# Performance work log

Measured on AMD Instinct MI355X. Metric: run time of the kernel, lower is better.

The kernel has to match this reference:

```python
import jax, jax.numpy as jnp
import numpy as np

N = 50000      # nodes
E = 800000     # edges (avg degree 16)
IN, HID, OUT = 128, 128, 64


def setup_inputs() -> dict:
    key = jax.random.key(0)
    ks = jax.random.split(key, 8)
    x = jax.random.normal(ks[0], (N, IN), dtype=jnp.float32)
    edge_index = jax.random.randint(ks[1], (2, E), 0, N, dtype=jnp.int64)
    s1 = 1.0 / np.sqrt(IN)
    s2 = 1.0 / np.sqrt(HID)
    # SAGEConv params: lin_l acts on aggregated neighbors (has bias), lin_r on root
    W1l = jax.random.uniform(ks[2], (IN, HID), jnp.float32, -s1, s1)
    W1r = jax.random.uniform(ks[3], (IN, HID), jnp.float32, -s1, s1)
    b1 = jax.random.uniform(ks[4], (HID,), jnp.float32, -s1, s1)
    W2l = jax.random.uniform(ks[5], (HID, OUT), jnp.float32, -s2, s2)
    W2r = jax.random.uniform(ks[6], (HID, OUT), jnp.float32, -s2, s2)
    b2 = jax.random.uniform(ks[7], (OUT,), jnp.float32, -s2, s2)
    return {"x": x, "edge_index": edge_index, "W1l": W1l, "W1r": W1r,
            "b1": b1, "W2l": W2l, "W2r": W2r, "b2": b2}


def reference(x, edge_index, W1l, W1r, b1, W2l, W2r, b2):
    src = edge_index[0]
    dst = edge_index[1]
    n = x.shape[0]
    deg = jax.ops.segment_sum(jnp.ones(src.shape, x.dtype), dst, num_segments=n)
    inv_deg = (1.0 / jnp.maximum(deg, 1.0))[:, None]  # [N,1], avoid div-by-zero

    def mean_agg(h):
        # gather neighbor feats, scatter-sum to destination, normalize by in-degree
        return jax.ops.segment_sum(h[src], dst, num_segments=n) * inv_deg

    # SAGEConv layer 1: lin_l(mean_j x_j) + lin_r(x_i), then ReLU (dropout off in eval)
    h = mean_agg(x) @ W1l + x @ W1r + b1
    h = jax.nn.relu(h)
    # SAGEConv layer 2
    out = mean_agg(h) @ W2l + h @ W2r + b2
    return out
```

## Files before the change

kernel.cpp:

```cpp
#include <hip/hip_runtime.h>
#include <hip/hip_bf16.h>


typedef __attribute__((ext_vector_type(8))) short bf16x8;
typedef __attribute__((ext_vector_type(4))) float f32x4;

__device__ __forceinline__ ushort f2b(float f) {
    uint u = __float_as_uint(f);
    return (ushort)((u + 0x7fffu + ((u >> 16) & 1u)) >> 16);
}
__device__ __forceinline__ float b2f(ushort h) { return __uint_as_float(((uint)h) << 16); }
__device__ __forceinline__ float blo(uint u) { return __uint_as_float(u << 16); }
__device__ __forceinline__ float bhi(uint u) { return __uint_as_float(u & 0xffff0000u); }

__global__ void count_deg_k(const int* __restrict__ dstv, int* __restrict__ cnt, int E) {
    int e = blockIdx.x * blockDim.x + threadIdx.x;
    if (e < E) atomicAdd(&cnt[dstv[e]], 1);
}

__global__ __launch_bounds__(256) void blocksum_k(const int* __restrict__ cnt,
                                                  int* __restrict__ bsum, int n) {
    __shared__ int red[4];
    int b = blockIdx.x, t = threadIdx.x;
    int base = b * 1024 + t * 4;
    int s = 0;
    #pragma unroll
    for (int i = 0; i < 4; ++i) { int idx = base + i; if (idx < n) s += cnt[idx]; }
    #pragma unroll
    for (int off = 32; off > 0; off >>= 1) s += __shfl_down(s, off);
    if ((t & 63) == 0) red[t >> 6] = s;
    __syncthreads();
    if (t == 0) bsum[b] = red[0] + red[1] + red[2] + red[3];
}

__global__ __launch_bounds__(256) void bscan_k(int* __restrict__ bsum, int nb) {
    __shared__ int sd[256];
    int t = threadIdx.x;
    int v = (t < nb) ? bsum[t] : 0;
    sd[t] = v;
    __syncthreads();
    for (int off = 1; off < 256; off <<= 1) {
        int u = (t >= off) ? sd[t - off] : 0;
        __syncthreads();
        sd[t] += u;
        __syncthreads();
    }
    if (t < nb) bsum[t] = sd[t] - v;
}

__global__ __launch_bounds__(256) void scanout_k(const int* __restrict__ cnt,
                                                 const int* __restrict__ bbase,
                                                 int* __restrict__ rowptr,
                                                 int* __restrict__ pos,
                                                 float* __restrict__ inv_deg,
                                                 int n, int E) {
    __shared__ int sums[256];
    int b = blockIdx.x, t = threadIdx.x;
    int base = b * 1024 + t * 4;
    int v[4];
    int s = 0;
    #pragma unroll
    for (int i = 0; i < 4; ++i) {
        int idx = base + i;
        v[i] = (idx < n) ? cnt[idx] : 0;
        s += v[i];
    }
    sums[t] = s;
    __syncthreads();
    for (int off = 1; off < 256; off <<= 1) {
        int u = (t >= off) ? sums[t - off] : 0;
        __syncthreads();
        sums[t] += u;
        __syncthreads();
    }
    int pre = sums[t] - s + bbase[b];
    #pragma unroll
    for (int i = 0; i < 4; ++i) {
        int idx = base + i;
        if (idx < n) {
            rowptr[idx] = pre;
            pos[idx] = pre;
            inv_deg[idx] = 1.0f / (float)max(v[i], 1);
            pre += v[i];
        }
    }
    if (b == 0 && t == 0) rowptr[n] = E;
}

__global__ void fill_k(const int* __restrict__ srcv, const int* __restrict__ dstv,
                       int* __restrict__ pos, int* __restrict__ csr, int E) {
    int e = blockIdx.x * blockDim.x + threadIdx.x;
    if (e < E) {
        int p = atomicAdd(&pos[dstv[e]], 1);
        csr[p] = srcv[e];
    }
}

__global__ void castx_k(const float* __restrict__ x, ushort* __restrict__ xb, int total4) {
    int i = blockIdx.x * blockDim.x + threadIdx.x;
    if (i < total4) {
        float4 v = reinterpret_cast<const float4*>(x)[i];
        ushort4 r;
        r.x = f2b(v.x); r.y = f2b(v.y); r.z = f2b(v.z); r.w = f2b(v.w);
        reinterpret_cast<ushort4*>(xb)[i] = r;
    }
}

__global__ void prepw_k(const float* __restrict__ W1l, const float* __restrict__ W1r,
                        const float* __restrict__ W2l, const float* __restrict__ W2r,
                        ushort* __restrict__ w1lt, ushort* __restrict__ w1rt,
                        ushort* __restrict__ w2lt, ushort* __restrict__ w2rt) {
    int i = blockIdx.x * blockDim.x + threadIdx.x;
    if (i < 16384) {
        int nn = i >> 7, k = i & 127;
        w1lt[i] = f2b(W1l[k * 128 + nn]);
    } else if (i < 32768) {
        int j = i - 16384, nn = j >> 7, k = j & 127;
        w1rt[j] = f2b(W1r[k * 128 + nn]);
    } else if (i < 40960) {
        int j = i - 32768, nn = j >> 7, k = j & 127;
        w2lt[j] = f2b(W2l[k * 64 + nn]);
    } else if (i < 49152) {
        int j = i - 40960, nn = j >> 7, k = j & 127;
        w2rt[j] = f2b(W2r[k * 64 + nn]);
    }
}

template<int F>
__global__ __launch_bounds__(256) void aggb_k(const ushort* __restrict__ feat,
                                              const int* __restrict__ rowptr,
                                              const int* __restrict__ csr,
                                              const float* __restrict__ invd,
                                              ushort* __restrict__ out, int n) {
    int tid = blockIdx.x * 256 + threadIdx.x;
    int node = tid >> 5;
    int sl = threadIdx.x & 31;
    if (node >= n) return;
    int s = rowptr[node], e = rowptr[node + 1];
    float sc = invd[node];
    if (F == 128) {
        float a0 = 0, a1 = 0, a2 = 0, a3 = 0;
        int p = s;
        for (; p + 2 <= e; p += 2) {
            int u0 = csr[p], u1 = csr[p + 1];
            uint2 v0 = *reinterpret_cast<const uint2*>(&feat[(size_t)u0 * 128 + sl * 4]);
            uint2 v1 = *reinterpret_cast<const uint2*>(&feat[(size_t)u1 * 128 + sl * 4]);
            a0 += blo(v0.x); a1 += bhi(v0.x); a2 += blo(v0.y); a3 += bhi(v0.y);
            a0 += blo(v1.x); a1 += bhi(v1.x); a2 += blo(v1.y); a3 += bhi(v1.y);
        }
        if (p < e) {
            uint2 v0 = *reinterpret_cast<const uint2*>(&feat[(size_t)csr[p] * 128 + sl * 4]);
            a0 += blo(v0.x); a1 += bhi(v0.x); a2 += blo(v0.y); a3 += bhi(v0.y);
        }
        ushort4 r;
        r.x = f2b(a0 * sc); r.y = f2b(a1 * sc); r.z = f2b(a2 * sc); r.w = f2b(a3 * sc);
        *reinterpret_cast<ushort4*>(&out[(size_t)node * 128 + sl * 4]) = r;
    } else {
        float a0 = 0, a1 = 0;
        int p = s;
        for (; p + 2 <= e; p += 2) {
            int u0 = csr[p], u1 = csr[p + 1];
            uint v0 = *reinterpret_cast<const uint*>(&feat[(size_t)u0 * 64 + sl * 2]);
            uint v1 = *reinterpret_cast<const uint*>(&feat[(size_t)u1 * 64 + sl * 2]);
            a0 += blo(v0) + blo(v1); a1 += bhi(v0) + bhi(v1);
        }
        if (p < e) {
            uint v0 = *reinterpret_cast<const uint*>(&feat[(size_t)csr[p] * 64 + sl * 2]);
            a0 += blo(v0); a1 += bhi(v0);
        }
        ushort2 r;
        r.x = f2b(a0 * sc); r.y = f2b(a1 * sc);
        *reinterpret_cast<ushort2*>(&out[(size_t)node * 64 + sl * 2]) = r;
    }
}

template<int NC, int NSRC, bool RELU, bool OUT_BF16, bool HAS_BIAS, bool HAS_ADD>
__global__ __launch_bounds__(256) void mgemm_k(const ushort* __restrict__ A0,
                                               const ushort* __restrict__ B0,
                                               const ushort* __restrict__ A1,
                                               const ushort* __restrict__ B1,
                                               const ushort* __restrict__ addm,
                                               const float* __restrict__ bias,
                                               void* __restrict__ Cout, int n) {
    constexpr int AST = 136;
    __shared__ ushort At[64 * AST];
    __shared__ ushort Bt[NC * AST];
    int t = threadIdx.x;
    int brow = blockIdx.x * 64;
    int w = t >> 6, l = t & 63, lrow = l & 15, lk = l >> 4;

    f32x4 acc[NC / 16];
    #pragma unroll
    for (int g = 0; g < NC / 16; ++g) acc[g] = (f32x4){0.f, 0.f, 0.f, 0.f};

    #pragma unroll
    for (int src = 0; src < NSRC; ++src) {
        const ushort* A = src ? A1 : A0;
        const ushort* B = src ? B1 : B0;
        __syncthreads();
        #pragma unroll
        for (int i = 0; i < 4; ++i) {
            int c = t + 256 * i, r = c >> 4, k16 = c & 15;
            int grow = brow + r;
            uint4 v = make_uint4(0, 0, 0, 0);
            if (grow < n) v = *reinterpret_cast<const uint4*>(&A[(size_t)grow * 128 + k16 * 8]);
            *reinterpret_cast<uint4*>(&At[r * AST + k16 * 8]) = v;
        }
        #pragma unroll
        for (int i = 0; i < NC / 16; ++i) {
            int c = t + 256 * i, r = c >> 4, k16 = c & 15;
            *reinterpret_cast<uint4*>(&Bt[r * AST + k16 * 8]) =
                *reinterpret_cast<const uint4*>(&B[(size_t)r * 128 + k16 * 8]);
        }
        __syncthreads();
        #pragma unroll
        for (int ks = 0; ks < 4; ++ks) {
            bf16x8 a = *reinterpret_cast<const bf16x8*>(&At[(w * 16 + lrow) * AST + ks * 32 + lk * 8]);
            #pragma unroll
            for (int g = 0; g < NC / 16; ++g) {
                bf16x8 b = *reinterpret_cast<const bf16x8*>(&Bt[(g * 16 + lrow) * AST + ks * 32 + lk * 8]);
                acc[g] = __builtin_amdgcn_mfma_f32_16x16x32_bf16(a, b, acc[g], 0, 0, 0);
            }
        }
    }

    int orow = brow + w * 16 + lk * 4;
    #pragma unroll
    for (int g = 0; g < NC / 16; ++g) {
        int gcol = g * 16 + lrow;
        float bv = HAS_BIAS ? bias[gcol] : 0.f;
        #pragma unroll
        for (int r = 0; r < 4; ++r) {
            int grow = orow + r;
            if (grow >= n) continue;
            float o = acc[g][r] + bv;
            if (HAS_ADD) o += b2f(addm[(size_t)grow * NC + gcol]);
            if (RELU) o = fmaxf(o, 0.f);
            if (OUT_BF16) ((ushort*)Cout)[(size_t)grow * NC + gcol] = f2b(o);
            else          ((float*)Cout)[(size_t)grow * NC + gcol] = o;
        }
    }
}

extern "C" void kernel_launch(void* const* d_in, const int* in_sizes, int n_in,
                              void* d_out, int out_size, void* d_ws, size_t ws_size,
                              hipStream_t stream) {
    const float* x   = (const float*)d_in[0];
    const int*   edge= (const int*)d_in[1];
    const float* W1l = (const float*)d_in[2];
    const float* W1r = (const float*)d_in[3];
    const float* b1  = (const float*)d_in[4];
    const float* W2l = (const float*)d_in[5];
    const float* W2r = (const float*)d_in[6];
    const float* b2  = (const float*)d_in[7];
    float* out = (float*)d_out;

    const int N = in_sizes[0] / 128;
    const int E = in_sizes[1] / 2;
    const int* srcv = edge;
    const int* dstv = edge + E;

    char* p = (char*)d_ws;
    auto alloc = [&](size_t bytes) {
        char* q = p;
        p += ((bytes + 255) & ~(size_t)255);
        return q;
    };
    int*    cnt    = (int*)alloc((size_t)N * 4);
    int*    rowptr = (int*)alloc((size_t)(N + 1) * 4);
    int*    pos    = (int*)alloc((size_t)N * 4);
    int*    csr    = (int*)alloc((size_t)E * 4);
    float*  invd   = (float*)alloc((size_t)N * 4);
    int*    bsum   = (int*)alloc((size_t)256 * 4);
    ushort* xb     = (ushort*)alloc((size_t)N * 128 * 2);
    ushort* tbuf   = (ushort*)alloc((size_t)N * 128 * 2);
    ushort* h      = (ushort*)alloc((size_t)N * 128 * 2);
    ushort* hl     = (ushort*)alloc((size_t)N * 64 * 2);
    ushort* t2     = (ushort*)alloc((size_t)N * 64 * 2);
    ushort* w1lt   = (ushort*)alloc((size_t)16384 * 2);
    ushort* w1rt   = (ushort*)alloc((size_t)16384 * 2);
    ushort* w2lt   = (ushort*)alloc((size_t)8192 * 2);
    ushort* w2rt   = (ushort*)alloc((size_t)8192 * 2);

    int nb = (N + 1023) / 1024;

    castx_k<<<(N * 32 + 255) / 256, 256, 0, stream>>>(x, xb, N * 32);
    prepw_k<<<192, 256, 0, stream>>>(W1l, W1r, W2l, W2r, w1lt, w1rt, w2lt, w2rt);

    hipMemsetAsync(cnt, 0, (size_t)N * 4, stream);
    count_deg_k<<<(E + 255) / 256, 256, 0, stream>>>(dstv, cnt, E);
    blocksum_k<<<nb, 256, 0, stream>>>(cnt, bsum, N);
    bscan_k<<<1, 256, 0, stream>>>(bsum, nb);
    scanout_k<<<nb, 256, 0, stream>>>(cnt, bsum, rowptr, pos, invd, N, E);
    fill_k<<<(E + 255) / 256, 256, 0, stream>>>(srcv, dstv, pos, csr, E);

    int gb = (N + 63) / 64;
    int ag = (N + 7) / 8;

    aggb_k<128><<<ag, 256, 0, stream>>>(xb, rowptr, csr, invd, tbuf, N);
    mgemm_k<128, 2, true, true, true, false><<<gb, 256, 0, stream>>>(
        xb, w1rt, tbuf, w1lt, nullptr, b1, h, N);
    mgemm_k<64, 1, false, true, false, false><<<gb, 256, 0, stream>>>(
        h, w2lt, nullptr, nullptr, nullptr, nullptr, hl, N);
    aggb_k<64><<<ag, 256, 0, stream>>>(hl, rowptr, csr, invd, t2, N);
    mgemm_k<64, 1, false, false, true, true><<<gb, 256, 0, stream>>>(
        h, w2rt, nullptr, nullptr, t2, b2, out, N);
}
```

Before: 290.2 us.

## Pre-bucket edges by destination range before CSR fill for locality

```diff
diff --git a/kernel.cpp b/kernel.cpp
--- a/kernel.cpp
+++ b/kernel.cpp
@@ -87,12 +87,52 @@
     if (b == 0 && t == 0) rowptr[n] = E;
 }
 
-__global__ void fill_k(const int* __restrict__ srcv, const int* __restrict__ dstv,
-                       int* __restrict__ pos, int* __restrict__ csr, int E) {
+__global__ void bucketbase_k(const int* __restrict__ rowptr, int* __restrict__ bucketPos,
+                             int nbuckets) {
+    int b = blockIdx.x * blockDim.x + threadIdx.x;
+    if (b < nbuckets) bucketPos[b] = rowptr[b * 256];
+}
+
+__global__ __launch_bounds__(256) void bucket_k(const int* __restrict__ srcv,
+                                                const int* __restrict__ dstv,
+                                                int* __restrict__ bucketPos,
+                                                uint2* __restrict__ ebuf, int E) {
+    __shared__ int hist[256], rbase[256];
+    int t = threadIdx.x;
+    int e0 = blockIdx.x * 2048;
+    hist[t] = 0;
+    __syncthreads();
+    int d[8], s[8];
+    #pragma unroll
+    for (int i = 0; i < 8; ++i) {
+        int e = e0 + t + 256 * i;
+        if (e < E) {
+            d[i] = dstv[e]; s[i] = srcv[e];
+            atomicAdd(&hist[d[i] >> 8], 1);
+        } else d[i] = -1;
+    }
+    __syncthreads();
+    if (hist[t] > 0) rbase[t] = atomicAdd(&bucketPos[t], hist[t]);
+    __syncthreads();
+    hist[t] = 0;
+    __syncthreads();
+    #pragma unroll
+    for (int i = 0; i < 8; ++i) {
+        if (d[i] >= 0) {
+            int b = d[i] >> 8;
+            int off = atomicAdd(&hist[b], 1);
+            ebuf[rbase[b] + off] = make_uint2((uint)d[i], (uint)s[i]);
+        }
+    }
+}
+
+__global__ void fill2_k(const uint2* __restrict__ ebuf, int* __restrict__ pos,
+                        int* __restrict__ csr, int E) {
     int e = blockIdx.x * blockDim.x + threadIdx.x;
     if (e < E) {
-        int p = atomicAdd(&pos[dstv[e]], 1);
-        csr[p] = srcv[e];
+        uint2 v = ebuf[e];
+        int p = atomicAdd(&pos[v.x], 1);
+        csr[p] = (int)v.y;
     }
 }
 
@@ -272,6 +312,8 @@
     int*    csr    = (int*)alloc((size_t)E * 4);
     float*  invd   = (float*)alloc((size_t)N * 4);
     int*    bsum   = (int*)alloc((size_t)256 * 4);
+    int*    bktpos = (int*)alloc((size_t)256 * 4);
+    uint2*  ebuf   = (uint2*)alloc((size_t)E * 8);
     ushort* xb     = (ushort*)alloc((size_t)N * 128 * 2);
     ushort* tbuf   = (ushort*)alloc((size_t)N * 128 * 2);
     ushort* h      = (ushort*)alloc((size_t)N * 128 * 2);
@@ -283,6 +325,7 @@
     ushort* w2rt   = (ushort*)alloc((size_t)8192 * 2);
 
     int nb = (N + 1023) / 1024;
+    int nbuckets = (N + 255) / 256;
 
     castx_k<<<(N * 32 + 255) / 256, 256, 0, stream>>>(x, xb, N * 32);
     prepw_k<<<192, 256, 0, stream>>>(W1l, W1r, W2l, W2r, w1lt, w1rt, w2lt, w2rt);
@@ -292,7 +335,9 @@
     blocksum_k<<<nb, 256, 0, stream>>>(cnt, bsum, N);
     bscan_k<<<1, 256, 0, stream>>>(bsum, nb);
     scanout_k<<<nb, 256, 0, stream>>>(cnt, bsum, rowptr, pos, invd, N, E);
-    fill_k<<<(E + 255) / 256, 256, 0, stream>>>(srcv, dstv, pos, csr, E);
+    bucketbase_k<<<1, 256, 0, stream>>>(rowptr, bktpos, nbuckets);
+    bucket_k<<<(E + 2047) / 2048, 256, 0, stream>>>(srcv, dstv, bktpos, ebuf, E);
+    fill2_k<<<(E + 255) / 256, 256, 0, stream>>>(ebuf, pos, csr, E);
 
     int gb = (N + 63) / 64;
     int ag = (N + 7) / 8;
```

Result: faster. 271.6 us (-6.4%).
